# Optimization experiments

Measured on AMD Instinct MI355X. Metric: run time of the kernel, lower is better.

Reference implementation:

```python
import jax, jax.numpy as jnp
import numpy as np

SPATIAL = [(100, 100), (50, 50), (25, 25), (13, 13)]
NUM_POINTS = [4, 4, 4, 4]
N_HEADS = 8
HIDDEN = 256
OFFSET_SCALE = 0.5

B, Q = 16, 300
S = sum(h * w for h, w in SPATIAL)


def setup_inputs() -> dict:
    key = jax.random.key(0)
    ks = jax.random.split(key, 7)
    total_points = N_HEADS * sum(NUM_POINTS)  # 128
    return {
        "hidden_states": jax.random.normal(ks[0], (B, Q, HIDDEN), jnp.float32),
        "encoder_hidden_states": jax.random.normal(ks[1], (B, S, HIDDEN), jnp.float32),
        "reference_points": jax.random.uniform(ks[2], (B, Q, 1, 4), jnp.float32),
        "W_off": jax.random.normal(ks[3], (HIDDEN, total_points * 2), jnp.float32) * 0.02,
        "b_off": jnp.zeros((total_points * 2,), jnp.float32),
        "W_attn": jax.random.normal(ks[4], (HIDDEN, total_points), jnp.float32) * 0.02,
        "b_attn": jnp.zeros((total_points,), jnp.float32),
    }


def _bilinear_sample(img, x, y, h, w):
    # img: [B, H, h, w, D]; x, y: [B, Q, H, P] pixel coords (align_corners=False)
    x0 = jnp.floor(x)
    y0 = jnp.floor(y)
    wx1 = x - x0
    wx0 = 1.0 - wx1
    wy1 = y - y0
    wy0 = 1.0 - wy1

    bi = jnp.arange(img.shape[0])[:, None, None, None]
    hi = jnp.arange(img.shape[1])[None, None, :, None]

    def gather(yy, xx):
        valid = (xx >= 0) & (xx <= w - 1) & (yy >= 0) & (yy <= h - 1)
        xi = jnp.clip(xx, 0, w - 1).astype(jnp.int32)
        yi = jnp.clip(yy, 0, h - 1).astype(jnp.int32)
        v = img[bi, hi, yi, xi]  # [B, Q, H, P, D]
        return v * valid[..., None].astype(img.dtype)

    return (gather(y0, x0) * (wy0 * wx0)[..., None]
            + gather(y0, x0 + 1) * (wy0 * wx1)[..., None]
            + gather(y0 + 1, x0) * (wy1 * wx0)[..., None]
            + gather(y0 + 1, x0 + 1) * (wy1 * wx1)[..., None])


def reference(hidden_states, encoder_hidden_states, reference_points, W_off, b_off, W_attn, b_attn):
    b, q, _ = hidden_states.shape
    s = encoder_hidden_states.shape[1]
    d = HIDDEN // N_HEADS
    p_total = sum(NUM_POINTS)

    # sampling offsets and attention weights projections
    off = (hidden_states @ W_off + b_off).reshape(b, q, N_HEADS, p_total, 2)
    aw = (hidden_states @ W_attn + b_attn).reshape(b, q, N_HEADS, p_total)
    aw = jax.nn.softmax(aw, axis=-1)

    # reference_points last dim == 4 branch
    scale = jnp.concatenate([jnp.full((n,), 1.0 / n, jnp.float32) for n in NUM_POINTS])
    offset = off * scale[:, None] * reference_points[..., 2:][:, :, :, None, :] * OFFSET_SCALE
    loc = reference_points[..., :2][:, :, :, None, :] + offset  # [B, Q, H, P, 2] in [0,1]

    value = encoder_hidden_states.reshape(b, s, N_HEADS, d)

    outs = []
    start, pstart = 0, 0
    for (h, w), n in zip(SPATIAL, NUM_POINTS):
        sz = h * w
        v = value[:, start:start + sz].reshape(b, h, w, N_HEADS, d).transpose(0, 3, 1, 2, 4)
        l = loc[:, :, :, pstart:pstart + n, :]
        # grid_sample align_corners=False: x = ((2*loc-1+1)*W - 1)/2 = loc*W - 0.5
        x = l[..., 0] * w - 0.5
        y = l[..., 1] * h - 0.5
        outs.append(_bilinear_sample(v, x, y, h, w))
        start += sz
        pstart += n

    sampled = jnp.concatenate(outs, axis=3)  # [B, Q, H, P_total, D]
    out = jnp.einsum('bqhpd,bqhp->bqhd', sampled, aw).reshape(b, q, HIDDEN)
    return out, aw
```

## Files before the change

kernel.cpp:

```cpp
#include <hip/hip_runtime.h>
#include <hip/hip_bf16.h>

#define B_      16
#define Q_      300
#define BQ      (B_*Q_)
#define HIDDEN_ 256
#define NHEADS  8
#define PTOT    16
#define S_      13294
#define NOFF    256
#define NATTN   128
#define NCOLS   (NOFF+NATTN)
#define OSTRIDE 388

typedef __attribute__((ext_vector_type(8))) short bf16x8;
typedef __attribute__((ext_vector_type(4))) float floatx4;

__device__ __forceinline__ short f2bf(float f) {
    unsigned u = __float_as_uint(f);
    unsigned r = (u + 0x7fffu + ((u >> 16) & 1u)) >> 16;
    return (short)r;
}

__global__ __launch_bounds__(256) void prep_kernel(
    const float* __restrict__ W_off,
    const float* __restrict__ W_attn,
    short* __restrict__ Wt)
{
    int id = blockIdx.x * 256 + threadIdx.x;
    int j = id >> 8;
    int k = id & 255;
    float v = (j < NOFF) ? W_off[k * NOFF + j] : W_attn[k * NATTN + (j - NOFF)];
    Wt[id] = f2bf(v);
}

__global__ __launch_bounds__(256) void proj_kernel(
    const float* __restrict__ hidden,
    const float* __restrict__ refp,
    const short* __restrict__ Wt,
    const float* __restrict__ b_off,
    const float* __restrict__ b_attn,
    float* __restrict__ aw_out,
    float* __restrict__ loc_out)
{
    __shared__ float o_s[16 * OSTRIDE];

    const int tid  = threadIdx.x;
    const int wave = tid >> 6;
    const int lane = tid & 63;
    const int m    = lane & 15;
    const int quad = lane >> 4;
    const int row0 = blockIdx.x * 16;

    floatx4 acc[6];
    #pragma unroll
    for (int i = 0; i < 6; ++i)
        #pragma unroll
        for (int r = 0; r < 4; ++r) acc[i][r] = 0.f;

    const float* hrow = hidden + (size_t)(row0 + m) * HIDDEN_;

    #pragma unroll
    for (int k0 = 0; k0 < HIDDEN_; k0 += 32) {
        const int kk = k0 + quad * 8;
        float4 a0 = *(const float4*)(hrow + kk);
        float4 a1 = *(const float4*)(hrow + kk + 4);
        bf16x8 af;
        af[0] = f2bf(a0.x); af[1] = f2bf(a0.y); af[2] = f2bf(a0.z); af[3] = f2bf(a0.w);
        af[4] = f2bf(a1.x); af[5] = f2bf(a1.y); af[6] = f2bf(a1.z); af[7] = f2bf(a1.w);
        #pragma unroll
        for (int i = 0; i < 6; ++i) {
            const int n0 = (wave * 6 + i) * 16;
            bf16x8 bf = *(const bf16x8*)(Wt + (size_t)(n0 + m) * HIDDEN_ + kk);
            acc[i] = __builtin_amdgcn_mfma_f32_16x16x32_bf16(af, bf, acc[i], 0, 0, 0);
        }
    }

    #pragma unroll
    for (int i = 0; i < 6; ++i) {
        const int n0  = (wave * 6 + i) * 16;
        const int col = n0 + m;
        const float bias = (col < NOFF) ? b_off[col] : b_attn[col - NOFF];
        #pragma unroll
        for (int r = 0; r < 4; ++r) {
            const int row = quad * 4 + r;
            o_s[row * OSTRIDE + col] = acc[i][r] + bias;
        }
    }
    __syncthreads();

    if (tid < 16 * NHEADS) {
        const int r  = tid >> 3;
        const int hd = tid & 7;
        const int row = row0 + r;

        float a[PTOT];
        float mx = -1e30f;
        #pragma unroll
        for (int p = 0; p < PTOT; ++p) {
            a[p] = o_s[r * OSTRIDE + NOFF + hd * PTOT + p];
            mx = fmaxf(mx, a[p]);
        }
        float s = 0.f;
        #pragma unroll
        for (int p = 0; p < PTOT; ++p) { a[p] = __expf(a[p] - mx); s += a[p]; }
        const float inv = 1.f / s;

        const float4 rp = ((const float4*)refp)[row];
        const float sx = 0.25f * rp.z * 0.5f;
        const float sy = 0.25f * rp.w * 0.5f;

        #pragma unroll
        for (int p = 0; p < PTOT; ++p) {
            const float awv = a[p] * inv;
            aw_out[row * NATTN + hd * PTOT + p] = awv;
            const float ox = o_s[r * OSTRIDE + (hd * PTOT + p) * 2];
            const float oy = o_s[r * OSTRIDE + (hd * PTOT + p) * 2 + 1];
            ((float2*)loc_out)[(row * NHEADS + hd) * PTOT + p] =
                make_float2(rp.x + ox * sx, rp.y + oy * sy);
        }
    }
}

__global__ __launch_bounds__(256) void sample_kernel(
    const float* __restrict__ enc,
    const float* __restrict__ aw,
    const float* __restrict__ loc,
    float* __restrict__ out)
{
    const int tid = threadIdx.x;
    const int g   = tid >> 6;
    const int l   = tid & 63;
    const int bq  = blockIdx.x * 4 + g;
    const int b   = bq / Q_;
    const int hd  = l >> 3;
    const int cq  = l & 7;

    __shared__ float  aw_s[4][NATTN];
    __shared__ float2 loc_s[4][NATTN];

    for (int i = tid; i < 4 * NATTN; i += 256)
        aw_s[i >> 7][i & 127] = aw[(size_t)(blockIdx.x * 4 + (i >> 7)) * NATTN + (i & 127)];
    for (int i = tid; i < 4 * NATTN * 2; i += 256)
        ((float*)loc_s)[i] = loc[(size_t)blockIdx.x * 4 * (NATTN * 2) + i];
    __syncthreads();

    const float4* encb = (const float4*)(enc + (size_t)b * S_ * HIDDEN_);
    const int c4 = hd * 8 + cq;

    float4 acc = make_float4(0.f, 0.f, 0.f, 0.f);

    #pragma unroll
    for (int p = 0; p < PTOT; ++p) {
        const int lvl   = p >> 2;
        const int Wl    = (lvl == 0) ? 100 : (lvl == 1) ? 50 : (lvl == 2) ? 25 : 13;
        const int start = (lvl == 0) ? 0 : (lvl == 1) ? 10000 : (lvl == 2) ? 12500 : 13125;

        const float2 lxy = loc_s[g][hd * PTOT + p];
        const float x = lxy.x * (float)Wl - 0.5f;
        const float y = lxy.y * (float)Wl - 0.5f;
        const float x0f = floorf(x), y0f = floorf(y);
        const float wx1 = x - x0f, wx0 = 1.f - wx1;
        const float wy1 = y - y0f, wy0 = 1.f - wy1;
        const int x0 = (int)x0f, y0 = (int)y0f;
        const int x1 = x0 + 1,  y1 = y0 + 1;

        const int x0c = x0 < 0 ? 0 : (x0 > Wl-1 ? Wl-1 : x0);
        const int x1c = x1 < 0 ? 0 : (x1 > Wl-1 ? Wl-1 : x1);
        const int y0c = y0 < 0 ? 0 : (y0 > Wl-1 ? Wl-1 : y0);
        const int y1c = y1 < 0 ? 0 : (y1 > Wl-1 ? Wl-1 : y1);
        const bool vx0 = (x0 >= 0) & (x0 <= Wl-1);
        const bool vx1 = (x1 >= 0) & (x1 <= Wl-1);
        const bool vy0 = (y0 >= 0) & (y0 <= Wl-1);
        const bool vy1 = (y1 >= 0) & (y1 <= Wl-1);

        const float w00 = (vy0 & vx0) ? wy0 * wx0 : 0.f;
        const float w01 = (vy0 & vx1) ? wy0 * wx1 : 0.f;
        const float w10 = (vy1 & vx0) ? wy1 * wx0 : 0.f;
        const float w11 = (vy1 & vx1) ? wy1 * wx1 : 0.f;

        const float4 v00 = encb[(size_t)(start + y0c * Wl + x0c) * 64 + c4];
        const float4 v01 = encb[(size_t)(start + y0c * Wl + x1c) * 64 + c4];
        const float4 v10 = encb[(size_t)(start + y1c * Wl + x0c) * 64 + c4];
        const float4 v11 = encb[(size_t)(start + y1c * Wl + x1c) * 64 + c4];

        float4 sm;
        sm.x = v00.x * w00 + v01.x * w01 + v10.x * w10 + v11.x * w11;
        sm.y = v00.y * w00 + v01.y * w01 + v10.y * w10 + v11.y * w11;
        sm.z = v00.z * w00 + v01.z * w01 + v10.z * w10 + v11.z * w11;
        sm.w = v00.w * w00 + v01.w * w01 + v10.w * w10 + v11.w * w11;

        const float a = aw_s[g][hd * PTOT + p];
        acc.x = fmaf(a, sm.x, acc.x);
        acc.y = fmaf(a, sm.y, acc.y);
        acc.z = fmaf(a, sm.z, acc.z);
        acc.w = fmaf(a, sm.w, acc.w);
    }

    *(float4*)(out + (size_t)bq * HIDDEN_ + l * 4) = acc;
}

extern "C" void kernel_launch(void* const* d_in, const int* in_sizes, int n_in,
                              void* d_out, int out_size, void* d_ws, size_t ws_size,
                              hipStream_t stream) {
    const float* hidden = (const float*)d_in[0];
    const float* enc    = (const float*)d_in[1];
    const float* refp   = (const float*)d_in[2];
    const float* W_off  = (const float*)d_in[3];
    const float* b_off  = (const float*)d_in[4];
    const float* W_attn = (const float*)d_in[5];
    const float* b_attn = (const float*)d_in[6];

    float* out    = (float*)d_out;
    float* aw_out = out + (size_t)BQ * HIDDEN_;

    short* Wt     = (short*)d_ws;
    float* loc_ws = (float*)d_ws + 65536;

    prep_kernel<<<NCOLS * HIDDEN_ / 256, 256, 0, stream>>>(W_off, W_attn, Wt);
    proj_kernel<<<BQ / 16, 256, 0, stream>>>(hidden, refp, Wt, b_off, b_attn, aw_out, loc_ws);
    sample_kernel<<<BQ / 4, 256, 0, stream>>>(enc, aw_out, loc_ws, out);
}
```

Measured before the change: 310.4 us.

## Remap sample blocks per XCD by batch and precompute gather tables in LDS

Measured after the change: 307.8 us. About the same (-0.8%).

```diff
diff --git a/kernel.cpp b/kernel.cpp
--- a/kernel.cpp
+++ b/kernel.cpp
@@ -12,6 +12,7 @@
 #define NATTN   128
 #define NCOLS   (NOFF+NATTN)
 #define OSTRIDE 388
+#define AS      264
 
 typedef __attribute__((ext_vector_type(8))) short bf16x8;
 typedef __attribute__((ext_vector_type(4))) float floatx4;
@@ -34,7 +35,7 @@
     Wt[id] = f2bf(v);
 }
 
-__global__ __launch_bounds__(256) void proj_kernel(
+__global__ __launch_bounds__(512) void proj_kernel(
     const float* __restrict__ hidden,
     const float* __restrict__ refp,
     const short* __restrict__ Wt,
@@ -43,6 +44,7 @@
     float* __restrict__ aw_out,
     float* __restrict__ loc_out)
 {
+    __shared__ short A_s[16 * AS];
     __shared__ float o_s[16 * OSTRIDE];
 
     const int tid  = threadIdx.x;
@@ -52,40 +54,45 @@
     const int quad = lane >> 4;
     const int row0 = blockIdx.x * 16;
 
-    floatx4 acc[6];
+    {
+        const int r  = tid >> 5;
+        const int ks = (tid & 31) * 8;
+        const float* hp = hidden + (size_t)(row0 + r) * HIDDEN_ + ks;
+        float4 a0 = *(const float4*)hp;
+        float4 a1 = *(const float4*)(hp + 4);
+        bf16x8 v;
+        v[0] = f2bf(a0.x); v[1] = f2bf(a0.y); v[2] = f2bf(a0.z); v[3] = f2bf(a0.w);
+        v[4] = f2bf(a1.x); v[5] = f2bf(a1.y); v[6] = f2bf(a1.z); v[7] = f2bf(a1.w);
+        *(bf16x8*)(A_s + r * AS + ks) = v;
+    }
+    __syncthreads();
+
+    floatx4 acc[3];
     #pragma unroll
-    for (int i = 0; i < 6; ++i)
+    for (int i = 0; i < 3; ++i)
         #pragma unroll
         for (int r = 0; r < 4; ++r) acc[i][r] = 0.f;
-
-    const float* hrow = hidden + (size_t)(row0 + m) * HIDDEN_;
 
     #pragma unroll
     for (int k0 = 0; k0 < HIDDEN_; k0 += 32) {
         const int kk = k0 + quad * 8;
-        float4 a0 = *(const float4*)(hrow + kk);
-        float4 a1 = *(const float4*)(hrow + kk + 4);
-        bf16x8 af;
-        af[0] = f2bf(a0.x); af[1] = f2bf(a0.y); af[2] = f2bf(a0.z); af[3] = f2bf(a0.w);
-        af[4] = f2bf(a1.x); af[5] = f2bf(a1.y); af[6] = f2bf(a1.z); af[7] = f2bf(a1.w);
-        #pragma unroll
-        for (int i = 0; i < 6; ++i) {
-            const int n0 = (wave * 6 + i) * 16;
+        bf16x8 af = *(const bf16x8*)(A_s + m * AS + kk);
+        #pragma unroll
+        for (int i = 0; i < 3; ++i) {
+            const int n0 = (wave * 3 + i) * 16;
             bf16x8 bf = *(const bf16x8*)(Wt + (size_t)(n0 + m) * HIDDEN_ + kk);
             acc[i] = __builtin_amdgcn_mfma_f32_16x16x32_bf16(af, bf, acc[i], 0, 0, 0);
         }
     }
 
     #pragma unroll
-    for (int i = 0; i < 6; ++i) {
-        const int n0  = (wave * 6 + i) * 16;
+    for (int i = 0; i < 3; ++i) {
+        const int n0  = (wave * 3 + i) * 16;
         const int col = n0 + m;
         const float bias = (col < NOFF) ? b_off[col] : b_attn[col - NOFF];
         #pragma unroll
-        for (int r = 0; r < 4; ++r) {
-            const int row = quad * 4 + r;
-            o_s[row * OSTRIDE + col] = acc[i][r] + bias;
-        }
+        for (int r = 0; r < 4; ++r)
+            o_s[(quad * 4 + r) * OSTRIDE + col] = acc[i][r] + bias;
     }
     __syncthreads();
 
@@ -128,35 +135,30 @@
     const float* __restrict__ loc,
     float* __restrict__ out)
 {
+    const int xcd = blockIdx.x & 7;
+    const int idx = blockIdx.x >> 3;
+    const int hi  = (idx >= 75);
+    const int bb  = xcd * 2 + hi;
+    const int qb  = idx - hi * 75;
+    const int bq0 = bb * Q_ + qb * 4;
+
+    __shared__ float2 tw_s[4 * NHEADS * PTOT * 4];
+
     const int tid = threadIdx.x;
-    const int g   = tid >> 6;
-    const int l   = tid & 63;
-    const int bq  = blockIdx.x * 4 + g;
-    const int b   = bq / Q_;
-    const int hd  = l >> 3;
-    const int cq  = l & 7;
-
-    __shared__ float  aw_s[4][NATTN];
-    __shared__ float2 loc_s[4][NATTN];
-
-    for (int i = tid; i < 4 * NATTN; i += 256)
-        aw_s[i >> 7][i & 127] = aw[(size_t)(blockIdx.x * 4 + (i >> 7)) * NATTN + (i & 127)];
-    for (int i = tid; i < 4 * NATTN * 2; i += 256)
-        ((float*)loc_s)[i] = loc[(size_t)blockIdx.x * 4 * (NATTN * 2) + i];
-    __syncthreads();
-
-    const float4* encb = (const float4*)(enc + (size_t)b * S_ * HIDDEN_);
-    const int c4 = hd * 8 + cq;
-
-    float4 acc = make_float4(0.f, 0.f, 0.f, 0.f);
-
-    #pragma unroll
-    for (int p = 0; p < PTOT; ++p) {
+
+    for (int t = tid; t < 4 * NHEADS * PTOT; t += 256) {
+        const int g    = t >> 7;
+        const int rest = t & 127;
+        const int p    = rest & 15;
+        const int bq   = bq0 + g;
+
+        const float2 lxy = ((const float2*)loc)[(size_t)bq * NATTN + rest];
+        const float  a   = aw[(size_t)bq * NATTN + rest];
+
         const int lvl   = p >> 2;
         const int Wl    = (lvl == 0) ? 100 : (lvl == 1) ? 50 : (lvl == 2) ? 25 : 13;
         const int start = (lvl == 0) ? 0 : (lvl == 1) ? 10000 : (lvl == 2) ? 12500 : 13125;
 
-        const float2 lxy = loc_s[g][hd * PTOT + p];
         const float x = lxy.x * (float)Wl - 0.5f;
         const float y = lxy.y * (float)Wl - 0.5f;
         const float x0f = floorf(x), y0f = floorf(y);
@@ -174,30 +176,44 @@
         const bool vy0 = (y0 >= 0) & (y0 <= Wl-1);
         const bool vy1 = (y1 >= 0) & (y1 <= Wl-1);
 
-        const float w00 = (vy0 & vx0) ? wy0 * wx0 : 0.f;
-        const float w01 = (vy0 & vx1) ? wy0 * wx1 : 0.f;
-        const float w10 = (vy1 & vx0) ? wy1 * wx0 : 0.f;
-        const float w11 = (vy1 & vx1) ? wy1 * wx1 : 0.f;
-
-        const float4 v00 = encb[(size_t)(start + y0c * Wl + x0c) * 64 + c4];
-        const float4 v01 = encb[(size_t)(start + y0c * Wl + x1c) * 64 + c4];
-        const float4 v10 = encb[(size_t)(start + y1c * Wl + x0c) * 64 + c4];
-        const float4 v11 = encb[(size_t)(start + y1c * Wl + x1c) * 64 + c4];
-
-        float4 sm;
-        sm.x = v00.x * w00 + v01.x * w01 + v10.x * w10 + v11.x * w11;
-        sm.y = v00.y * w00 + v01.y * w01 + v10.y * w10 + v11.y * w11;
-        sm.z = v00.z * w00 + v01.z * w01 + v10.z * w10 + v11.z * w11;
-        sm.w = v00.w * w00 + v01.w * w01 + v10.w * w10 + v11.w * w11;
-
-        const float a = aw_s[g][hd * PTOT + p];
-        acc.x = fmaf(a, sm.x, acc.x);
-        acc.y = fmaf(a, sm.y, acc.y);
-        acc.z = fmaf(a, sm.z, acc.z);
-        acc.w = fmaf(a, sm.w, acc.w);
-    }
-
-    *(float4*)(out + (size_t)bq * HIDDEN_ + l * 4) = acc;
+        const int r00 = start + y0c * Wl + x0c;
+        const int r01 = start + y0c * Wl + x1c;
+        const int r10 = start + y1c * Wl + x0c;
+        const int r11 = start + y1c * Wl + x1c;
+
+        float2* dst = &tw_s[t * 4];
+        dst[0] = make_float2(__int_as_float(r00), (vy0 & vx0) ? a * wy0 * wx0 : 0.f);
+        dst[1] = make_float2(__int_as_float(r01), (vy0 & vx1) ? a * wy0 * wx1 : 0.f);
+        dst[2] = make_float2(__int_as_float(r10), (vy1 & vx0) ? a * wy1 * wx0 : 0.f);
+        dst[3] = make_float2(__int_as_float(r11), (vy1 & vx1) ? a * wy1 * wx1 : 0.f);
+    }
+    __syncthreads();
+
+    const int g    = tid >> 6;
+    const int lane = tid & 63;
+    const int hd   = lane >> 3;
+    const int cq   = lane & 7;
+    const int bq   = bq0 + g;
+
+    const float4* encb = (const float4*)(enc + (size_t)bb * S_ * HIDDEN_);
+    const int c4   = hd * 8 + cq;
+    const int base = (g * NHEADS + hd) * PTOT * 4;
+
+    float4 acc = make_float4(0.f, 0.f, 0.f, 0.f);
+
+    #pragma unroll 16
+    for (int i = 0; i < PTOT * 4; ++i) {
+        const float2 tw = tw_s[base + i];
+        const int row = __float_as_int(tw.x);
+        const float w = tw.y;
+        const float4 v = encb[(size_t)row * 64 + c4];
+        acc.x = fmaf(w, v.x, acc.x);
+        acc.y = fmaf(w, v.y, acc.y);
+        acc.z = fmaf(w, v.z, acc.z);
+        acc.w = fmaf(w, v.w, acc.w);
+    }
+
+    ((float4*)out)[(size_t)bq * 64 + c4] = acc;
 }
 
 extern "C" void kernel_launch(void* const* d_in, const int* in_sizes, int n_in,
@@ -218,6 +234,6 @@
     float* loc_ws = (float*)d_ws + 65536;
 
     prep_kernel<<<NCOLS * HIDDEN_ / 256, 256, 0, stream>>>(W_off, W_attn, Wt);
-    proj_kernel<<<BQ / 16, 256, 0, stream>>>(hidden, refp, Wt, b_off, b_attn, aw_out, loc_ws);
+    proj_kernel<<<BQ / 16, 512, 0, stream>>>(hidden, refp, Wt, b_off, b_attn, aw_out, loc_ws);
     sample_kernel<<<BQ / 4, 256, 0, stream>>>(enc, aw_out, loc_ws, out);
 }
```
